# Performance work log

Measured on AMD Instinct MI355X. Metric: run time of the kernel, lower is better.

## Reference

```python
import jax, jax.numpy as jnp
import numpy as np

B, TE, TD = 16, 400, 64
E, H = 256, 512
H2 = 2 * H  # 1024
V = 32000


def setup_inputs():
    key = jax.random.key(0)
    k = jax.random.split(key, 16)
    s = 0.05
    return {
        "encoder_inputs": jax.random.randint(k[0], (B, TE), 0, V),
        "decoder_inputs": jax.random.randint(k[1], (B, TD), 0, V),
        "ext_oov_sizes": jax.random.randint(k[2], (B,), 0, 10),
        "enc_idxes_on_ext_voc": jax.random.randint(k[3], (B, TE), 0, V),
        "h0": jnp.zeros((2, B, H), jnp.float32),
        "c0": jnp.zeros((2, B, H), jnp.float32),
        "emb": jax.random.normal(k[4], (V, E)) * 0.1,
        "Wih_f": jax.random.normal(k[5], (4 * H, E)) * s,
        "Whh_f": jax.random.normal(k[6], (4 * H, H)) * s,
        "b_f": jnp.zeros((4 * H,), jnp.float32),
        "Wih_b": jax.random.normal(k[7], (4 * H, E)) * s,
        "Whh_b": jax.random.normal(k[8], (4 * H, H)) * s,
        "b_b": jnp.zeros((4 * H,), jnp.float32),
        "Wih_d": jax.random.normal(k[9], (4 * H2, E + 2 * H2)) * s,
        "Whh_d": jax.random.normal(k[10], (4 * H2, H2)) * s,
        "b_d": jnp.zeros((4 * H2,), jnp.float32),
        "W_ea": jax.random.normal(k[11], (H2, H2)) * 0.006,
        "W_da": jax.random.normal(k[12], (H2, H2)) * 0.006,
        "W_v": jax.random.normal(k[13], (V, 3 * H2)) * s,
        "b_v": jnp.zeros((V,), jnp.float32),
    }


def lstm_cell(x, h, c, Wih, Whh, b):
    z = x @ Wih.T + h @ Whh.T + b
    i, f, g, o = jnp.split(z, 4, axis=-1)
    i, f, o = jax.nn.sigmoid(i), jax.nn.sigmoid(f), jax.nn.sigmoid(o)
    c2 = f * c + i * jnp.tanh(g)
    return o * jnp.tanh(c2), c2


def run_lstm(xs, h0, c0, Wih, Whh, b):
    # xs: [T, B, E]
    def step(carry, x):
        h, c = lstm_cell(x, carry[0], carry[1], Wih, Whh, b)
        return (h, c), h
    (h, c), hs = jax.lax.scan(step, (h0, c0), xs)
    return hs, h, c


def _forward(emb, Wih_f, Whh_f, b_f, Wih_b, Whh_b, b_b, Wih_d, Whh_d, b_d,
             W_ea, W_da, W_v, b_v, h0, c0, encoder_inputs, decoder_inputs):
    xs = emb[encoder_inputs].transpose(1, 0, 2)  # [TE, B, E]
    hs_f, hf, cf = run_lstm(xs, h0[0], c0[0], Wih_f, Whh_f, b_f)
    hs_b, hb, cb = run_lstm(xs[::-1], h0[1], c0[1], Wih_b, Whh_b, b_b)
    enc_out = jnp.concatenate([hs_f, hs_b[::-1]], axis=-1).transpose(1, 0, 2)  # [B, TE, 2H]
    h = jnp.concatenate([hf, hb], axis=-1)  # [B, 2H] (torch reshape of bi-dir last hidden)
    c = jnp.concatenate([cf, cb], axis=-1)
    dec_emb = emb[decoder_inputs].transpose(1, 0, 2)  # [TD, B, E]

    def step(carry, xs_t):
        h, c, accum, buf = carry
        i, emb_t = xs_t
        # intra-temporal encoder attention: exp scores normalized by past accumulation
        scores = jnp.einsum('bd,btd->bt', h @ W_ea, enc_out)  # [B, TE]
        exp_s = jnp.exp(scores)
        denom = jnp.where(i == 0, jnp.ones_like(accum), accum)
        ep = exp_s / denom
        attn = ep / jnp.sum(ep, axis=-1, keepdims=True)
        ctx_e = jnp.einsum('bt,btd->bd', attn, enc_out)
        # intra-decoder attention over previously produced hidden states (masked)
        dsc = jnp.einsum('bd,tbd->bt', h @ W_da, buf)  # [B, TD]
        dsc = jnp.where((jnp.arange(TD) < i)[None, :], dsc, -1e30)
        dw = jnp.where(i == 0, 0.0, jax.nn.softmax(dsc, axis=-1))
        ctx_d = jnp.einsum('bt,tbd->bd', dw, buf)
        x = jnp.concatenate([emb_t, ctx_e, ctx_d], axis=-1)  # [B, E+4H]
        h2, c2 = lstm_cell(x, h, c, Wih_d, Whh_d, b_d)
        buf2 = buf.at[i].set(h2)
        feat = jnp.concatenate([h2, ctx_e, ctx_d], axis=-1)  # [B, 6H]
        logd = jax.nn.log_softmax(feat @ W_v.T + b_v, axis=-1)
        return (h2, c2, accum + exp_s, buf2), logd

    carry0 = (h, c, jnp.zeros((B, TE), h.dtype), jnp.zeros((TD, B, H2), h.dtype))
    (h, c, _, _), logds = jax.lax.scan(step, carry0, (jnp.arange(TD), dec_emb))
    return logds.transpose(1, 0, 2), h[None], c[None]


def reference(encoder_inputs, decoder_inputs, ext_oov_sizes, enc_idxes_on_ext_voc,
              h0, c0, emb, Wih_f, Whh_f, b_f, Wih_b, Whh_b, b_b,
              Wih_d, Whh_d, b_d, W_ea, W_da, W_v, b_v):
    # ext_oov_sizes / enc_idxes_on_ext_voc are unused by forward (as in the torch source)
    return _forward(emb, Wih_f, Whh_f, b_f, Wih_b, Whh_b, b_b, Wih_d, Whh_d, b_d,
                    W_ea, W_da, W_v, b_v, h0, c0, encoder_inputs, decoder_inputs)
```

## Files before the change

### kernel.cpp

```cpp
#include <hip/hip_runtime.h>
#include <math.h>

#define B_  16
#define TE_ 400
#define TD_ 64
#define E_  256
#define H_  512
#define H2_ 1024
#define V_  32000
#define KE_ 768

typedef __attribute__((ext_vector_type(4))) float f32x4;
typedef __attribute__((ext_vector_type(8))) short s16x8;
typedef __attribute__((ext_vector_type(8))) unsigned short u16x8;
typedef __attribute__((ext_vector_type(4))) unsigned short u16x4;

__device__ __forceinline__ float bf2f(unsigned short u){
  union { unsigned int i; float f; } v; v.i = ((unsigned int)u) << 16; return v.f;
}
__device__ __forceinline__ unsigned short f2bf(float f){
  union { float f; unsigned int i; } v; v.f = f;
  return (unsigned short)((v.i + 0x7fffu + ((v.i >> 16) & 1u)) >> 16);
}
__device__ __forceinline__ float sigmoidf_(float x){ return 1.f/(1.f + expf(-x)); }

__device__ __forceinline__ void gl_lds16(const void* gsrc, void* ldst){
  __builtin_amdgcn_global_load_lds(
      (const __attribute__((address_space(1))) unsigned int*)gsrc,
      (__attribute__((address_space(3))) unsigned int*)ldst, 16, 0, 0);
}

__device__ __forceinline__ void bar_arrive(unsigned* obj, unsigned widx){
  __syncthreads();
  if (threadIdx.x == 0){
    __threadfence();
    __hip_atomic_fetch_add(&obj[(widx & 7u)*32], 1u, __ATOMIC_RELAXED, __HIP_MEMORY_SCOPE_AGENT);
  }
}
__device__ __forceinline__ void bar_wait(unsigned* obj, unsigned nwg, unsigned widx, unsigned epoch){
  if (threadIdx.x == 0){
    if (widx == 0){
      for(;;){
        unsigned s = 0;
        #pragma unroll
        for (int k2 = 0; k2 < 8; ++k2)
          s += __hip_atomic_load(&obj[k2*32], __ATOMIC_RELAXED, __HIP_MEMORY_SCOPE_AGENT);
        if (s >= nwg*epoch) break;
      }
      __hip_atomic_store(&obj[256], epoch, __ATOMIC_RELEASE, __HIP_MEMORY_SCOPE_AGENT);
    } else {
      while (__hip_atomic_load(&obj[256], __ATOMIC_RELAXED, __HIP_MEMORY_SCOPE_AGENT) < epoch)
        __builtin_amdgcn_s_sleep(1);
    }
    __threadfence();
  }
  __syncthreads();
}
__device__ __forceinline__ void fast_bar(unsigned* obj, unsigned nwg, unsigned widx, unsigned epoch){
  bar_arrive(obj, widx);
  bar_wait(obj, nwg, widx, epoch);
}

__global__ void k_init(unsigned* bars, float* accum){
  int gid = blockIdx.x*256 + threadIdx.x;
  if (gid < 4096) bars[gid] = 0u;
  if (gid < B_*TE_) accum[gid] = 0.f;
}

__global__ void k_gather(const float* __restrict__ emb, const int* __restrict__ idx,
                         unsigned short* __restrict__ out, int T){
  int wv = threadIdx.x >> 6, l = threadIdx.x & 63;
  int row = blockIdx.x*4 + wv;
  if (row >= T*B_) return;
  int t = row >> 4, b = row & 15;
  int tok = idx[b*T + t];
  float4 v = *(const float4*)(emb + (size_t)tok*E_ + l*4);
  u16x4 o; o[0]=f2bf(v.x); o[1]=f2bf(v.y); o[2]=f2bf(v.z); o[3]=f2bf(v.w);
  *(u16x4*)(out + (size_t)row*E_ + l*4) = o;
}

__global__ void k_prep_enc(const float* __restrict__ Wih_f, const float* __restrict__ Whh_f,
                           const float* __restrict__ Wih_b, const float* __restrict__ Whh_b,
                           unsigned short* __restrict__ Wenc){
  int it = blockIdx.x*256 + threadIdx.x;
  int dir = it / (2048*96); int rem = it % (2048*96);
  int pr = rem / 96; int kc = rem % 96; int k0 = kc*8;
  int g = pr >> 6, r = pr & 63, gate = r >> 4, ul = r & 15;
  int orig = gate*H_ + g*16 + ul;
  const float* Wih = dir ? Wih_b : Wih_f;
  const float* Whh = dir ? Whh_b : Whh_f;
  u16x8 o;
  #pragma unroll
  for (int e = 0; e < 8; ++e){
    int k = k0 + e;
    float v = (k < E_) ? Wih[(size_t)orig*E_ + k] : Whh[(size_t)orig*H_ + (k - E_)];
    o[e] = f2bf(v);
  }
  *(u16x8*)(Wenc + ((size_t)dir*2048 + pr)*KE_ + k0) = o;
}

__global__ void k_prep_whext(const float* __restrict__ Whh_d, const float* __restrict__ W_da,
                             char* __restrict__ WhExt){
  int it = blockIdx.x*256 + threadIdx.x;
  if (it < 524288){
    int g = it >> 13; int rem = it & 8191;
    int kblk = rem >> 10; int rem2 = rem & 1023;
    int row = rem2 >> 4; int k8 = rem2 & 15;
    int gate = row >> 4, ul = row & 15;
    int orig = gate*H2_ + g*16 + ul;
    u16x8 o;
    #pragma unroll
    for (int e = 0; e < 8; ++e)
      o[e] = f2bf(Whh_d[(size_t)orig*H2_ + kblk*128 + k8*8 + e]);
    size_t off = (size_t)g*163840 + (size_t)kblk*20480 + (size_t)(row*256 + ((k8*16) ^ ((row&7)<<4)));
    *(u16x8*)(WhExt + off) = o;
  } else if (it < 655360){
    int qi = it - 524288;
    int g = qi >> 11; int rem = qi & 2047;
    int kblk = rem >> 8; int c2 = rem & 255;
    int wv = c2 >> 6, rr = (c2 >> 2) & 15, c = c2 & 3;
    u16x8 o;
    #pragma unroll
    for (int e = 0; e < 8; ++e)
      o[e] = f2bf(W_da[(size_t)(g*16 + rr)*H2_ + kblk*128 + wv*32 + c*8 + e]);
    size_t off = (size_t)g*163840 + (size_t)kblk*20480 + 16384 + (size_t)(wv*1024 + rr*64 + ((c*16) ^ ((rr&7)<<4)));
    *(u16x8*)(WhExt + off) = o;
  }
}

__global__ void k_prep_ctx(const float* __restrict__ Wih_d, char* __restrict__ CtxW){
  int it = blockIdx.x*256 + threadIdx.x;
  int g = it >> 14; int rem = it & 16383;
  int kblk = rem >> 10; int rem2 = rem & 1023;
  int row = rem2 >> 4; int k8 = rem2 & 15;
  int gate = row >> 4, ul = row & 15;
  int orig = gate*H2_ + g*16 + ul;
  int k = 256 + kblk*128 + k8*8;
  u16x8 o;
  #pragma unroll
  for (int e = 0; e < 8; ++e)
    o[e] = f2bf(Wih_d[(size_t)orig*2304 + k + e]);
  size_t off = (size_t)g*262144 + (size_t)kblk*16384 + (size_t)(row*256 + ((k8*16) ^ ((row&7)<<4)));
  *(u16x8*)(CtxW + off) = o;
}

__global__ void k_prep_wihemb(const float* __restrict__ Wih_d, unsigned short* __restrict__ Wemb){
  int it = blockIdx.x*256 + threadIdx.x;
  int p = it >> 5; int k0 = (it & 31)*8;
  int g = p >> 6, gate = (p >> 4) & 3, ul = p & 15;
  int orig = gate*H2_ + g*16 + ul;
  u16x8 o;
  #pragma unroll
  for (int e = 0; e < 8; ++e)
    o[e] = f2bf(Wih_d[(size_t)orig*2304 + k0 + e]);
  *(u16x8*)(Wemb + (size_t)p*256 + k0) = o;
}

__global__ void __launch_bounds__(256, 2) k_zinit(
    const unsigned short* __restrict__ A,
    const unsigned short* __restrict__ Bw,
    const float* __restrict__ bd,
    float* __restrict__ Cz)
{
  __shared__ unsigned short Ab[128*72];
  __shared__ unsigned short Bt[128*72];
  int p = blockIdx.x;
  int mt = p >> 5, nt = p & 31;
  int m0 = mt*128, n0 = nt*128;
  int tid = threadIdx.x, wvv = tid>>6, l = tid&63;
  int wr = wvv>>1, wc = wvv&1;
  f32x4 zero4 = {0.f,0.f,0.f,0.f};
  f32x4 acc[4][4];
  #pragma unroll
  for (int a=0;a<4;++a){
    #pragma unroll
    for (int b=0;b<4;++b) acc[a][b] = zero4;
  }
  for (int k0 = 0; k0 < 256; k0 += 64){
    #pragma unroll
    for (int qq = 0; qq < 4; ++qq){
      int idx8 = (tid + qq*256)*8;
      int r = idx8 >> 6, k = idx8 & 63;
      *(u16x8*)(Ab + r*72 + k) = *(const u16x8*)(A + (size_t)(m0+r)*256 + k0 + k);
      *(u16x8*)(Bt + r*72 + k) = *(const u16x8*)(Bw + (size_t)(n0+r)*256 + k0 + k);
    }
    __syncthreads();
    #pragma unroll
    for (int ks = 0; ks < 2; ++ks){
      s16x8 af[4], bf[4];
      #pragma unroll
      for (int fi=0;fi<4;++fi)
        af[fi] = *(const s16x8*)(Ab + (wr*64+fi*16+(l&15))*72 + ks*32 + (l>>4)*8);
      #pragma unroll
      for (int fj=0;fj<4;++fj)
        bf[fj] = *(const s16x8*)(Bt + (wc*64+fj*16+(l&15))*72 + ks*32 + (l>>4)*8);
      #pragma unroll
      for (int fi=0;fi<4;++fi){
        #pragma unroll
        for (int fj=0;fj<4;++fj)
          acc[fi][fj] = __builtin_amdgcn_mfma_f32_16x16x32_bf16(af[fi], bf[fj], acc[fi][fj], 0,0,0);
      }
    }
    __syncthreads();
  }
  #pragma unroll
  for (int fj=0;fj<4;++fj){
    int col = n0 + wc*64 + fj*16 + (l&15);
    int orig = ((col>>4)&3)*H2_ + (col>>6)*16 + (col&15);
    float bias = bd[orig];
    #pragma unroll
    for (int fi=0;fi<4;++fi){
      #pragma unroll
      for (int j=0;j<4;++j){
        int row = m0 + wr*64 + fi*16 + (l>>4)*4 + j;
        Cz[(size_t)row*4096 + col] = acc[fi][fj][j] + bias;
      }
    }
  }
}

__global__ void __launch_bounds__(256, 1) k_encoder(
    const unsigned short* __restrict__ xs,
    const unsigned short* __restrict__ Wenc,
    const float* __restrict__ b_f, const float* __restrict__ b_b,
    const float* __restrict__ h0, const float* __restrict__ c0,
    unsigned short* __restrict__ enc_out,
    unsigned short* __restrict__ hbuf,
    float* __restrict__ h0dec, float* __restrict__ c0dec,
    unsigned* __restrict__ bars)
{
  extern __shared__ char smem[];
  unsigned short* Wt = (unsigned short*)smem;
  unsigned short* At = Wt + 64*776;
  float* zl = (float*)(At + 16*776);
  int tid = threadIdx.x;
  int w = blockIdx.x;
  int dir = w >> 5, g = w & 31;
  int wv = tid >> 6, l = tid & 63;
  unsigned* bobj = bars + dir*512;
  {
    const unsigned short* Wsrc = Wenc + ((size_t)dir*2048 + g*64)*KE_;
    int r = tid >> 2, s = tid & 3;
    for (int c = 0; c < 24; ++c)
      *(u16x8*)(Wt + r*776 + s*192 + c*8) = *(const u16x8*)(Wsrc + (size_t)r*KE_ + s*192 + c*8);
  }
  const float* bias = dir ? b_b : b_f;
  int bb = tid >> 4, ul = tid & 15;
  float creg = c0[((size_t)dir*16 + bb)*H_ + g*16 + ul];
  int kchunk = (l >> 4) * 8;
  float bia = bias[wv*H_ + g*16 + (l&15)];
  f32x4 bias4 = { bia, bia, bia, bia };
  f32x4 zero4 = { 0.f, 0.f, 0.f, 0.f };
  {
    int r = tid >> 4, s = tid & 15;
    int tg0 = dir ? (TE_-1) : 0;
    *(u16x8*)(At + r*776 + s*16)     = *(const u16x8*)(xs + ((size_t)tg0*16 + r)*E_ + s*16);
    *(u16x8*)(At + r*776 + s*16 + 8) = *(const u16x8*)(xs + ((size_t)tg0*16 + r)*E_ + s*16 + 8);
    for (int e = 0; e < 32; ++e)
      At[r*776 + 256 + s*32 + e] = f2bf(h0[((size_t)dir*16 + r)*H_ + s*32 + e]);
  }
  __syncthreads();
  for (int t = 0; t < TE_; ++t){
    int tg = dir ? (TE_-1 - t) : t;
    f32x4 acc0 = bias4, acc1 = zero4;
    const unsigned short* brow = Wt + (wv*16 + (l&15))*776 + kchunk;
    const unsigned short* ap   = At + (l&15)*776 + kchunk;
    #pragma unroll
    for (int ks = 0; ks < 24; ++ks){
      s16x8 afr = *(const s16x8*)(ap + ks*32);
      s16x8 bfr = *(const s16x8*)(brow + ks*32);
      if (ks & 1) acc1 = __builtin_amdgcn_mfma_f32_16x16x32_bf16(afr, bfr, acc1, 0, 0, 0);
      else        acc0 = __builtin_amdgcn_mfma_f32_16x16x32_bf16(afr, bfr, acc0, 0, 0, 0);
    }
    f32x4 acc = acc0 + acc1;
    #pragma unroll
    for (int j = 0; j < 4; ++j)
      zl[wv*256 + ((l>>4)*4 + j)*16 + (l&15)] = acc[j];
    __syncthreads();
    float zi = zl[0*256 + bb*16 + ul];
    float zf = zl[1*256 + bb*16 + ul];
    float zg = zl[2*256 + bb*16 + ul];
    float zo = zl[3*256 + bb*16 + ul];
    float iv = sigmoidf_(zi), fv = sigmoidf_(zf), gv = tanhf(zg), ov = sigmoidf_(zo);
    float cc = fv*creg + iv*gv;
    float hh = ov * tanhf(cc);
    creg = cc;
    int u = g*16 + ul;
    unsigned short hb = f2bf(hh);
    hbuf[((size_t)dir*2 + ((t+1)&1))*(16*H_) + bb*H_ + u] = hb;
    enc_out[((size_t)bb*TE_ + tg)*H2_ + dir*H_ + u] = hb;
    if (t == TE_-1){
      h0dec[(size_t)bb*H2_ + dir*H_ + u] = hh;
      c0dec[(size_t)bb*H2_ + dir*H_ + u] = cc;
    }
    bar_arrive(bobj, (unsigned)g);
    if (t+1 < TE_){
      int r = tid >> 4, s = tid & 15;
      int tg2 = dir ? (TE_-2 - t) : (t+1);
      *(u16x8*)(At + r*776 + s*16)     = *(const u16x8*)(xs + ((size_t)tg2*16 + r)*E_ + s*16);
      *(u16x8*)(At + r*776 + s*16 + 8) = *(const u16x8*)(xs + ((size_t)tg2*16 + r)*E_ + s*16 + 8);
    }
    bar_wait(bobj, 32, (unsigned)g, (unsigned)(t+1));
    if (t+1 < TE_){
      int r = tid >> 4, s = tid & 15;
      const unsigned short* hsrc = hbuf + ((size_t)dir*2 + ((t+1)&1))*(16*H_) + r*H_ + s*32;
      for (int c = 0; c < 4; ++c)
        *(u16x8*)(At + r*776 + 256 + s*32 + c*8) = *(const u16x8*)(hsrc + c*8);
    }
    __syncthreads();
  }
}

__global__ void k_dec_init(const float* __restrict__ h0dec, unsigned short* __restrict__ hreg){
  int gid = blockIdx.x*256 + threadIdx.x;
  if (gid < 16384) hreg[gid] = f2bf(h0dec[gid]);
}

__global__ void __launch_bounds__(256, 2) k_penc(
    const unsigned short* __restrict__ enc,
    const float* __restrict__ Wea,
    unsigned short* __restrict__ P)
{
  __shared__ unsigned short Ab[128*72];
  __shared__ unsigned short Bt[128*72];
  int p = blockIdx.x;
  int mt = p >> 3, nt = p & 7;
  int m0 = mt*128, n0 = nt*128;
  int tid = threadIdx.x, wvv = tid>>6, l = tid&63;
  int wr = wvv>>1, wc = wvv&1;
  f32x4 zero4 = {0.f,0.f,0.f,0.f};
  f32x4 acc[4][4];
  #pragma unroll
  for (int a=0;a<4;++a){
    #pragma unroll
    for (int b=0;b<4;++b) acc[a][b] = zero4;
  }
  for (int k0 = 0; k0 < 1024; k0 += 64){
    #pragma unroll
    for (int qq = 0; qq < 4; ++qq){
      int idx8 = (tid + qq*256)*8;
      int r = idx8 >> 6, k = idx8 & 63;
      *(u16x8*)(Ab + r*72 + k) = *(const u16x8*)(enc + (size_t)(m0+r)*1024 + k0 + k);
    }
    #pragma unroll
    for (int qq = 0; qq < 4; ++qq){
      int idx8 = (tid + qq*256)*8;
      int r = idx8 >> 6, k = idx8 & 63;
      const float* src = Wea + (size_t)(n0+r)*1024 + k0 + k;
      float4 v0 = *(const float4*)src;
      float4 v1 = *(const float4*)(src+4);
      u16x8 o;
      o[0]=f2bf(v0.x); o[1]=f2bf(v0.y); o[2]=f2bf(v0.z); o[3]=f2bf(v0.w);
      o[4]=f2bf(v1.x); o[5]=f2bf(v1.y); o[6]=f2bf(v1.z); o[7]=f2bf(v1.w);
      *(u16x8*)(Bt + r*72 + k) = o;
    }
    __syncthreads();
    #pragma unroll
    for (int ks = 0; ks < 2; ++ks){
      s16x8 af[4], bf[4];
      #pragma unroll
      for (int fi=0;fi<4;++fi)
        af[fi] = *(const s16x8*)(Ab + (wr*64+fi*16+(l&15))*72 + ks*32 + (l>>4)*8);
      #pragma unroll
      for (int fj=0;fj<4;++fj)
        bf[fj] = *(const s16x8*)(Bt + (wc*64+fj*16+(l&15))*72 + ks*32 + (l>>4)*8);
      #pragma unroll
      for (int fi=0;fi<4;++fi){
        #pragma unroll
        for (int fj=0;fj<4;++fj)
          acc[fi][fj] = __builtin_amdgcn_mfma_f32_16x16x32_bf16(af[fi], bf[fj], acc[fi][fj], 0,0,0);
      }
    }
    __syncthreads();
  }
  #pragma unroll
  for (int fj=0;fj<4;++fj){
    int col = n0 + wc*64 + fj*16 + (l&15);
    #pragma unroll
    for (int fi=0;fi<4;++fi){
      #pragma unroll
      for (int j=0;j<4;++j){
        int row = m0 + wr*64 + fi*16 + (l>>4)*4 + j;
        P[(size_t)row*1024 + col] = f2bf(acc[fi][fj][j]);
      }
    }
  }
}

__device__ __forceinline__ void issueA(const char* gA, char* Bb, int wv, int l, int kblk, int buf){
  const char* gsrc = gA + (size_t)kblk*20480;
  char* lb = Bb + buf*20480;
  #pragma unroll
  for (int q = 0; q < 4; ++q)
    gl_lds16(gsrc + wv*4096 + q*1024 + (size_t)l*16, lb + wv*4096 + q*1024);
  gl_lds16(gsrc + 16384 + wv*1024 + (size_t)l*16, lb + 16384 + wv*1024);
}
__device__ __forceinline__ void issueC(const char* gC, char* Bb, int wv, int l, int kblk, int buf){
  const char* gsrc = gC + (size_t)kblk*16384;
  char* lb = Bb + buf*20480;
  #pragma unroll
  for (int q = 0; q < 4; ++q)
    gl_lds16(gsrc + wv*4096 + q*1024 + (size_t)l*16, lb + wv*4096 + q*1024);
}

__global__ void __launch_bounds__(256, 1) k_decoder(
  const char* __restrict__ WhExt,
  const char* __restrict__ CtxW,
  const float* __restrict__ zinit,
  const unsigned short* __restrict__ Penc,
  const unsigned short* __restrict__ enc_out,
  const float* __restrict__ c0dec,
  unsigned short* __restrict__ hreg,
  unsigned short* __restrict__ xbuf,
  float* __restrict__ q,
  float* __restrict__ accum,
  float* __restrict__ pctx,
  float* __restrict__ psum,
  unsigned short* __restrict__ bufh,
  unsigned short* __restrict__ Av,
  float* __restrict__ outHC,
  unsigned* __restrict__ bars)
{
  extern __shared__ char smem[];
  int tid = threadIdx.x, w = blockIdx.x;
  int wv = tid >> 6, l = tid & 63;
  unsigned* objA = bars + 1024;
  unsigned* objB = bars + 1536;
  unsigned* objC = bars + 2048;

  unsigned short* Atc = (unsigned short*)smem;
  unsigned short* Ah  = (unsigned short*)smem;
  char*  Bb = smem + 66560;
  float* zl = (float*)(smem + 148480);
  float* zq = (float*)(smem + 152576);
  unsigned short* encL = (unsigned short*)smem;
  float* epL  = (float*)(smem + 102400);
  float* dscL = (float*)(smem + 103424);

  bool isL = (w < 64);
  int eb = 0, ec = 0;
  if (w >= 64){ eb = (w-64) >> 3; ec = (w-64) & 7; }

  if (w >= 64){
    for (int rr = 0; rr < 50; ++rr){
      const unsigned short* src = enc_out + ((size_t)eb*TE_ + ec*50 + rr)*H2_;
      *(u16x4*)(encL + rr*1024 + tid*4) = *(const u16x4*)(src + tid*4);
    }
    __syncthreads();
  }
  float creg = 0.f;
  int bb = tid >> 4, ul = tid & 15;
  const char* gA = (const char*)WhExt + (size_t)w*163840;
  const char* gC = (const char*)CtxW + (size_t)w*262144;

  f32x4 acc0, acc1;

  for (int i = 0; i < TD_; ++i){
    if (isL){
      issueA(gA, Bb, wv, l, 0, 0);
      issueA(gA, Bb, wv, l, 1, 1);
      {
        int r = tid >> 4, s = tid & 15;
        const unsigned short* hsrc = hreg + (i&1)*16384 + r*H2_ + s*64;
        for (int c = 0; c < 8; ++c)
          *(u16x8*)(Ah + r*1032 + s*64 + c*8) = *(const u16x8*)(hsrc + c*8);
      }
      __syncthreads();
      {
        const float* zsrc = zinit + ((size_t)i*16 + (l>>4)*4)*4096 + w*64 + wv*16 + (l&15);
        f32x4 a; a[0]=zsrc[0]; a[1]=zsrc[4096]; a[2]=zsrc[8192]; a[3]=zsrc[12288];
        acc0 = a;
        f32x4 z4 = {0.f,0.f,0.f,0.f};
        acc1 = z4;
      }
      f32x4 accq = {0.f,0.f,0.f,0.f};
      int swz = ((l&7)<<4);
      for (int kblk = 0; kblk < 8; ++kblk){
        int buf = kblk % 3;
        if (kblk + 2 < 8) issueA(gA, Bb, wv, l, kblk+2, (kblk+2)%3);
        if (kblk < 6)       asm volatile("s_waitcnt vmcnt(10)" ::: "memory");
        else if (kblk == 6) asm volatile("s_waitcnt vmcnt(5)" ::: "memory");
        else                asm volatile("s_waitcnt vmcnt(0)" ::: "memory");
        const unsigned short* ap = Ah + (l&15)*1032 + kblk*128 + (l>>4)*8;
        const char* Bz = Bb + buf*20480 + wv*4096;
        #pragma unroll
        for (int ks = 0; ks < 4; ++ks){
          int k8 = ks*4 + (l>>4);
          s16x8 afr = *(const s16x8*)(ap + ks*32);
          s16x8 bfr = *(const s16x8*)(Bz + (l&15)*256 + ((k8*16) ^ swz));
          if (ks & 1) acc1 = __builtin_amdgcn_mfma_f32_16x16x32_bf16(afr, bfr, acc1, 0,0,0);
          else        acc0 = __builtin_amdgcn_mfma_f32_16x16x32_bf16(afr, bfr, acc0, 0,0,0);
        }
        {
          s16x8 afq = *(const s16x8*)(Ah + (l&15)*1032 + kblk*128 + wv*32 + (l>>4)*8);
          s16x8 bfq = *(const s16x8*)(Bb + buf*20480 + 16384 + wv*1024 + (l&15)*64 + ((((l>>4)*16)) ^ swz));
          accq = __builtin_amdgcn_mfma_f32_16x16x32_bf16(afq, bfq, accq, 0,0,0);
        }
      }
      #pragma unroll
      for (int j = 0; j < 4; ++j)
        zq[wv*256 + ((l>>4)*4+j)*16 + (l&15)] = accq[j];
      __syncthreads();
      float qv = zq[0*256 + bb*16 + ul] + zq[1*256 + bb*16 + ul]
               + zq[2*256 + bb*16 + ul] + zq[3*256 + bb*16 + ul];
      q[(size_t)bb*H2_ + w*16 + ul] = qv;
    } else {
      const unsigned short* hb_ = hreg + (i&1)*16384 + eb*H2_ + l*16;
      u16x8 hv0 = *(const u16x8*)hb_;
      u16x8 hv1 = *(const u16x8*)(hb_ + 8);
      float hf[16];
      #pragma unroll
      for (int c = 0; c < 8; ++c){ hf[c] = bf2f(hv0[c]); hf[8+c] = bf2f(hv1[c]); }
      for (int rr = wv; rr < 50; rr += 4){
        const unsigned short* pr = Penc + ((size_t)(eb*TE_ + ec*50 + rr))*H2_ + l*16;
        u16x8 p0 = *(const u16x8*)pr;
        u16x8 p1 = *(const u16x8*)(pr + 8);
        float sc = 0.f;
        #pragma unroll
        for (int c = 0; c < 8; ++c) sc += hf[c]*bf2f(p0[c]);
        #pragma unroll
        for (int c = 0; c < 8; ++c) sc += hf[8+c]*bf2f(p1[c]);
        #pragma unroll
        for (int o = 1; o < 64; o <<= 1) sc += __shfl_xor(sc, o);
        if (l == 0){
          int t = ec*50 + rr;
          float es = expf(sc);
          float aold = accum[eb*TE_ + t];
          float denom = (i == 0) ? 1.f : aold;
          accum[eb*TE_ + t] = aold + es;
          epL[rr] = es / denom;
        }
      }
      __syncthreads();
      float tot = 0.f;
      for (int rr = 0; rr < 50; ++rr) tot += epL[rr];
      float a0=0.f,a1=0.f,a2=0.f,a3=0.f;
      for (int rr = 0; rr < 50; ++rr){
        float wgt = epL[rr];
        u16x4 ev = *(const u16x4*)(encL + rr*1024 + tid*4);
        a0 += wgt*bf2f(ev[0]); a1 += wgt*bf2f(ev[1]); a2 += wgt*bf2f(ev[2]); a3 += wgt*bf2f(ev[3]);
      }
      int slot = w - 64;
      float4 o4; o4.x=a0; o4.y=a1; o4.z=a2; o4.w=a3;
      *(float4*)(pctx + (size_t)slot*1024 + tid*4) = o4;
      if (tid == 0) psum[slot] = tot;
      __syncthreads();
    }
    fast_bar(objA, 192, (unsigned)w, (unsigned)(i+1));

    if (isL){
      #pragma unroll
      for (int j = 0; j < 4; ++j)
        issueC(gC, Bb, wv, l, j, j);
    } else if (w < 96){
      int b = (w-64) >> 1, half = w & 1;
      int col = half*512 + tid*2;
      if (i == 0){
        *(unsigned*)(xbuf + (size_t)b*2048 + 1024 + col) = 0u;
        *(unsigned*)(Av + ((size_t)b*TD_ + i)*3072 + 2048 + col) = 0u;
      } else {
        const float* qp = q + (size_t)b*H2_ + l*16;
        float4 q0 = *(const float4*)(qp);
        float4 q1 = *(const float4*)(qp+4);
        float4 q2 = *(const float4*)(qp+8);
        float4 q3 = *(const float4*)(qp+12);
        for (int tp = wv; tp < i; tp += 4){
          const unsigned short* br = bufh + ((size_t)tp*16 + b)*H2_ + l*16;
          u16x8 e0 = *(const u16x8*)(br);
          u16x8 e1 = *(const u16x8*)(br + 8);
          float sc = q0.x*bf2f(e0[0]) + q0.y*bf2f(e0[1]) + q0.z*bf2f(e0[2]) + q0.w*bf2f(e0[3])
                   + q1.x*bf2f(e0[4]) + q1.y*bf2f(e0[5]) + q1.z*bf2f(e0[6]) + q1.w*bf2f(e0[7])
                   + q2.x*bf2f(e1[0]) + q2.y*bf2f(e1[1]) + q2.z*bf2f(e1[2]) + q2.w*bf2f(e1[3])
                   + q3.x*bf2f(e1[4]) + q3.y*bf2f(e1[5]) + q3.z*bf2f(e1[6]) + q3.w*bf2f(e1[7]);
          #pragma unroll
          for (int o = 1; o < 64; o <<= 1) sc += __shfl_xor(sc, o);
          if (l == 0) dscL[tp] = sc;
        }
        __syncthreads();
        float scv = (l < i) ? dscL[l] : -1e30f;
        float m = scv;
        #pragma unroll
        for (int o = 1; o < 64; o <<= 1) m = fmaxf(m, __shfl_xor(m, o));
        float e = (l < i) ? expf(scv - m) : 0.f;
        float ssum = e;
        #pragma unroll
        for (int o = 1; o < 64; o <<= 1) ssum += __shfl_xor(ssum, o);
        float wgt = e / ssum;
        float c0_ = 0.f, c1_ = 0.f;
        for (int tp = 0; tp < i; ++tp){
          float wt = __shfl(wgt, tp);
          unsigned hv = *(const unsigned*)(bufh + ((size_t)tp*16 + b)*H2_ + col);
          c0_ += wt*bf2f((unsigned short)hv);
          c1_ += wt*bf2f((unsigned short)(hv>>16));
        }
        unsigned o2 = (unsigned)f2bf(c0_) | ((unsigned)f2bf(c1_) << 16);
        *(unsigned*)(xbuf + (size_t)b*2048 + 1024 + col) = o2;
        *(unsigned*)(Av + ((size_t)b*TD_ + i)*3072 + 2048 + col) = o2;
      }
    } else if (w < 112){
      int b = w - 96;
      float sx=0.f, sy=0.f, sz=0.f, sw=0.f, pst=0.f;
      for (int c = 0; c < 8; ++c){
        float4 v = *(const float4*)(pctx + (size_t)(b*8+c)*1024 + tid*4);
        sx += v.x; sy += v.y; sz += v.z; sw += v.w;
        pst += psum[b*8+c];
      }
      float inv = 1.f/pst;
      u16x4 o; o[0]=f2bf(sx*inv); o[1]=f2bf(sy*inv); o[2]=f2bf(sz*inv); o[3]=f2bf(sw*inv);
      *(u16x4*)(xbuf + (size_t)b*2048 + tid*4) = o;
      *(u16x4*)(Av + ((size_t)b*TD_ + i)*3072 + 1024 + tid*4) = o;
    }
    fast_bar(objB, 192, (unsigned)w, (unsigned)(i+1));

    if (isL){
      {
        int r = tid >> 4, s = tid & 15;
        for (int c = 0; c < 16; ++c)
          *(u16x8*)(Atc + r*2056 + s*128 + c*8) = *(const u16x8*)(xbuf + (size_t)r*2048 + s*128 + c*8);
      }
      __syncthreads();
      int swz = ((l&7)<<4);
      for (int kblk = 0; kblk < 16; ++kblk){
        int buf = kblk & 3;
        if (kblk >= 4 && kblk <= 12) asm volatile("s_waitcnt vmcnt(12)" ::: "memory");
        else if (kblk == 13)         asm volatile("s_waitcnt vmcnt(8)" ::: "memory");
        else if (kblk == 14)         asm volatile("s_waitcnt vmcnt(4)" ::: "memory");
        else if (kblk == 15)         asm volatile("s_waitcnt vmcnt(0)" ::: "memory");
        const unsigned short* ap = Atc + (l&15)*2056 + kblk*128 + (l>>4)*8;
        const char* Bz = Bb + buf*20480 + wv*4096;
        #pragma unroll
        for (int ks = 0; ks < 4; ++ks){
          int k8 = ks*4 + (l>>4);
          s16x8 afr = *(const s16x8*)(ap + ks*32);
          s16x8 bfr = *(const s16x8*)(Bz + (l&15)*256 + ((k8*16) ^ swz));
          if (ks & 1) acc1 = __builtin_amdgcn_mfma_f32_16x16x32_bf16(afr, bfr, acc1, 0,0,0);
          else        acc0 = __builtin_amdgcn_mfma_f32_16x16x32_bf16(afr, bfr, acc0, 0,0,0);
        }
        if (kblk + 4 < 16) issueC(gC, Bb, wv, l, kblk+4, buf);
      }
      f32x4 acc = acc0 + acc1;
      #pragma unroll
      for (int j = 0; j < 4; ++j)
        zl[wv*256 + ((l>>4)*4+j)*16 + (l&15)] = acc[j];
      __syncthreads();
      float zi = zl[0*256 + bb*16 + ul];
      float zf = zl[1*256 + bb*16 + ul];
      float zg = zl[2*256 + bb*16 + ul];
      float zo = zl[3*256 + bb*16 + ul];
      if (i == 0) creg = c0dec[(size_t)bb*H2_ + w*16 + ul];
      float iv = sigmoidf_(zi), fv = sigmoidf_(zf), gv = tanhf(zg), ov = sigmoidf_(zo);
      float cc = fv*creg + iv*gv;
      float hh = ov*tanhf(cc);
      creg = cc;
      int u = w*16 + ul;
      unsigned short hb2 = f2bf(hh);
      hreg[((i+1)&1)*16384 + (size_t)bb*H2_ + u] = hb2;
      Av[((size_t)bb*TD_ + i)*3072 + u] = hb2;
      bufh[((size_t)i*16 + bb)*H2_ + u] = hb2;
      if (i == TD_-1){
        outHC[(size_t)bb*H2_ + u] = hh;
        outHC[16384 + (size_t)bb*H2_ + u] = cc;
      }
    }
    fast_bar(objC, 192, (unsigned)w, (unsigned)(i+1));
  }
}

__global__ void __launch_bounds__(256, 2) k_vocab_gemm(
    const unsigned short* __restrict__ Av,
    const float* __restrict__ Wv,
    const float* __restrict__ bv,
    float* __restrict__ out)
{
  __shared__ unsigned short Ab[128*72];
  __shared__ unsigned short Bt[128*72];
  int p = blockIdx.x;
  int mt = (p>>3)&7, nt = (p&7) + 8*(p>>6);
  if (nt >= 250) return;
  int m0 = mt*128, n0 = nt*128;
  int tid = threadIdx.x, wvv = tid>>6, l = tid&63;
  int wr = wvv>>1, wc = wvv&1;
  f32x4 zero4 = {0.f,0.f,0.f,0.f};
  f32x4 acc[4][4];
  #pragma unroll
  for (int a=0;a<4;++a){
    #pragma unroll
    for (int b=0;b<4;++b) acc[a][b] = zero4;
  }
  for (int k0 = 0; k0 < 3072; k0 += 64){
    #pragma unroll
    for (int qq = 0; qq < 4; ++qq){
      int idx8 = (tid + qq*256)*8;
      int r = idx8 >> 6, k = idx8 & 63;
      *(u16x8*)(Ab + r*72 + k) = *(const u16x8*)(Av + (size_t)(m0+r)*3072 + k0 + k);
    }
    #pragma unroll
    for (int qq = 0; qq < 4; ++qq){
      int idx8 = (tid + qq*256)*8;
      int r = idx8 >> 6, k = idx8 & 63;
      const float* src = Wv + (size_t)(n0+r)*3072 + k0 + k;
      float4 v0 = *(const float4*)src;
      float4 v1 = *(const float4*)(src+4);
      u16x8 o;
      o[0]=f2bf(v0.x); o[1]=f2bf(v0.y); o[2]=f2bf(v0.z); o[3]=f2bf(v0.w);
      o[4]=f2bf(v1.x); o[5]=f2bf(v1.y); o[6]=f2bf(v1.z); o[7]=f2bf(v1.w);
      *(u16x8*)(Bt + r*72 + k) = o;
    }
    __syncthreads();
    #pragma unroll
    for (int ks = 0; ks < 2; ++ks){
      s16x8 af[4], bf[4];
      #pragma unroll
      for (int fi=0;fi<4;++fi)
        af[fi] = *(const s16x8*)(Ab + (wr*64+fi*16+(l&15))*72 + ks*32 + (l>>4)*8);
      #pragma unroll
      for (int fj=0;fj<4;++fj)
        bf[fj] = *(const s16x8*)(Bt + (wc*64+fj*16+(l&15))*72 + ks*32 + (l>>4)*8);
      #pragma unroll
      for (int fi=0;fi<4;++fi){
        #pragma unroll
        for (int fj=0;fj<4;++fj)
          acc[fi][fj] = __builtin_amdgcn_mfma_f32_16x16x32_bf16(af[fi], bf[fj], acc[fi][fj], 0,0,0);
      }
    }
    __syncthreads();
  }
  #pragma unroll
  for (int fj=0;fj<4;++fj){
    int col = n0 + wc*64 + fj*16 + (l&15);
    float bias = bv[col];
    #pragma unroll
    for (int fi=0;fi<4;++fi){
      #pragma unroll
      for (int j=0;j<4;++j){
        int row = m0 + wr*64 + fi*16 + (l>>4)*4 + j;
        out[(size_t)row*V_ + col] = acc[fi][fj][j] + bias;
      }
    }
  }
}

__global__ void k_logsoftmax(float* __restrict__ out){
  int row = blockIdx.x;
  float* x = out + (size_t)row*V_;
  int tid = threadIdx.x;
  __shared__ float red[64];
  float m = -1e30f;
  for (int c = tid; c < V_; c += 256) m = fmaxf(m, x[c]);
  #pragma unroll
  for (int o=1;o<64;o<<=1) m = fmaxf(m, __shfl_xor(m,o));
  if ((tid&63)==0) red[tid>>6] = m;
  __syncthreads();
  m = fmaxf(fmaxf(red[0],red[1]), fmaxf(red[2],red[3]));
  float s = 0.f;
  for (int c = tid; c < V_; c += 256) s += expf(x[c]-m);
  #pragma unroll
  for (int o=1;o<64;o<<=1) s += __shfl_xor(s,o);
  if ((tid&63)==0) red[8 + (tid>>6)] = s;
  __syncthreads();
  s = red[8]+red[9]+red[10]+red[11];
  float lse = m + logf(s);
  for (int c = tid; c < V_; c += 256) x[c] = x[c] - lse;
}

extern "C" void kernel_launch(void* const* d_in, const int* in_sizes, int n_in,
                              void* d_out, int out_size, void* d_ws, size_t ws_size,
                              hipStream_t stream){
  (void)in_sizes; (void)n_in; (void)out_size; (void)ws_size;
  const int*   enc_in = (const int*)d_in[0];
  const int*   dec_in = (const int*)d_in[1];
  const float* h0   = (const float*)d_in[4];
  const float* c0   = (const float*)d_in[5];
  const float* emb  = (const float*)d_in[6];
  const float* Wih_f= (const float*)d_in[7];
  const float* Whh_f= (const float*)d_in[8];
  const float* b_f  = (const float*)d_in[9];
  const float* Wih_b= (const float*)d_in[10];
  const float* Whh_b= (const float*)d_in[11];
  const float* b_b  = (const float*)d_in[12];
  const float* Wih_d= (const float*)d_in[13];
  const float* Whh_d= (const float*)d_in[14];
  const float* b_d  = (const float*)d_in[15];
  const float* W_ea = (const float*)d_in[16];
  const float* W_da = (const float*)d_in[17];
  const float* W_v  = (const float*)d_in[18];
  const float* b_v  = (const float*)d_in[19];
  float* out = (float*)d_out;
  char* ws = (char*)d_ws;

  size_t o_bars   = 0;
  size_t o_accum  = 16384;
  size_t o_q      = o_accum + 25600;
  size_t o_xs     = o_q + 65536;
  size_t o_decemb = o_xs + (size_t)6400*256*2;
  size_t o_Wenc   = o_decemb + (size_t)1024*256*2;
  size_t o_WhExt  = o_Wenc + (size_t)2*2048*768*2;
  size_t o_CtxW   = o_WhExt + (size_t)64*163840;
  size_t o_Wemb   = o_CtxW + (size_t)64*262144;
  size_t o_zinit  = o_Wemb + (size_t)4096*256*2;
  size_t o_enc    = o_zinit + (size_t)1024*4096*4;
  size_t o_Penc   = o_enc + (size_t)16*400*1024*2;
  size_t o_hbuf   = o_Penc + (size_t)16*400*1024*2;
  size_t o_h0dec  = o_hbuf + (size_t)2*2*16*512*2;
  size_t o_c0dec  = o_h0dec + (size_t)16*1024*4;
  size_t o_hreg   = o_c0dec + (size_t)16*1024*4;
  size_t o_xbuf   = o_hreg + (size_t)2*16*1024*2;
  size_t o_pctx   = o_xbuf + (size_t)16*2048*2;
  size_t o_psum   = o_pctx + (size_t)128*1024*4;
  size_t o_bufh   = o_psum + 512;
  size_t o_Av     = o_bufh + (size_t)64*16*1024*2;

  unsigned* bars        = (unsigned*)(ws + o_bars);
  float* accum          = (float*)(ws + o_accum);
  float* q              = (float*)(ws + o_q);
  unsigned short* xs    = (unsigned short*)(ws + o_xs);
  unsigned short* decemb= (unsigned short*)(ws + o_decemb);
  unsigned short* Wenc  = (unsigned short*)(ws + o_Wenc);
  char* WhExt           = ws + o_WhExt;
  char* CtxW            = ws + o_CtxW;
  unsigned short* Wemb  = (unsigned short*)(ws + o_Wemb);
  float* zinit          = (float*)(ws + o_zinit);
  unsigned short* encO  = (unsigned short*)(ws + o_enc);
  unsigned short* Penc  = (unsigned short*)(ws + o_Penc);
  unsigned short* hbuf  = (unsigned short*)(ws + o_hbuf);
  float* h0dec          = (float*)(ws + o_h0dec);
  float* c0dec          = (float*)(ws + o_c0dec);
  unsigned short* hreg  = (unsigned short*)(ws + o_hreg);
  unsigned short* xbuf  = (unsigned short*)(ws + o_xbuf);
  float* pctx           = (float*)(ws + o_pctx);
  float* psum           = (float*)(ws + o_psum);
  unsigned short* bufh  = (unsigned short*)(ws + o_bufh);
  unsigned short* Av    = (unsigned short*)(ws + o_Av);

  hipFuncSetAttribute((const void*)k_encoder, hipFuncAttributeMaxDynamicSharedMemorySize, 131072);
  hipFuncSetAttribute((const void*)k_decoder, hipFuncAttributeMaxDynamicSharedMemorySize, 157696);

  k_init<<<26, 256, 0, stream>>>(bars, accum);
  k_gather<<<1600, 256, 0, stream>>>(emb, enc_in, xs, TE_);
  k_gather<<<256, 256, 0, stream>>>(emb, dec_in, decemb, TD_);
  k_prep_enc<<<1536, 256, 0, stream>>>(Wih_f, Whh_f, Wih_b, Whh_b, Wenc);
  k_prep_whext<<<2560, 256, 0, stream>>>(Whh_d, W_da, WhExt);
  k_prep_ctx<<<4096, 256, 0, stream>>>(Wih_d, CtxW);
  k_prep_wihemb<<<512, 256, 0, stream>>>(Wih_d, Wemb);
  k_zinit<<<256, 256, 0, stream>>>(decemb, Wemb, b_d, zinit);
  k_encoder<<<64, 256, 128512, stream>>>(xs, Wenc, b_f, b_b, h0, c0, encO, hbuf, h0dec, c0dec, bars);
  k_penc<<<400, 256, 0, stream>>>(encO, W_ea, Penc);
  k_dec_init<<<64, 256, 0, stream>>>(h0dec, hreg);
  k_decoder<<<192, 256, 156672, stream>>>(WhExt, CtxW, zinit, Penc, encO, c0dec,
                                          hreg, xbuf, q, accum, pctx, psum, bufh, Av,
                                          out + (size_t)32768000, bars);
  k_vocab_gemm<<<2048, 256, 0, stream>>>(Av, W_v, b_v, out);
  k_logsoftmax<<<1024, 256, 0, stream>>>(out);
}
```

Before: 6.342 ms.

## Fold encoder attention projection into decoder query, overlap weight prep with encoder

Removes the separate Penc GEMM over encoder outputs and instead projects the decoder state through W_ea each step, so attention scores are computed as enc_out·(W_ea^T·q). Weight-repacking kernels are folded into spare blocks of the encoder launch, which gets extra idle blocks so the packing overlaps the serial encoder recurrence. The encoder's and decoder's grid barriers are replaced with per-step counter barriers that need no reset. The context vector is accumulated atomically into a normalized buffer instead of a separate reduction phase. This trades a large up-front GEMM and extra launches for more per-step decoder work and more complex synchronization.

Measured after the change: 6.222 ms. Within noise of the previous version (-1.9%).

```diff
diff --git a/kernel.cpp b/kernel.cpp
--- a/kernel.cpp
+++ b/kernel.cpp
@@ -30,41 +30,30 @@
       (__attribute__((address_space(3))) unsigned int*)ldst, 16, 0, 0);
 }
 
-__device__ __forceinline__ void bar_arrive(unsigned* obj, unsigned widx){
+__device__ __forceinline__ void dec_bar(unsigned* inst, unsigned nwg){
   __syncthreads();
   if (threadIdx.x == 0){
     __threadfence();
-    __hip_atomic_fetch_add(&obj[(widx & 7u)*32], 1u, __ATOMIC_RELAXED, __HIP_MEMORY_SCOPE_AGENT);
-  }
-}
-__device__ __forceinline__ void bar_wait(unsigned* obj, unsigned nwg, unsigned widx, unsigned epoch){
-  if (threadIdx.x == 0){
-    if (widx == 0){
-      for(;;){
-        unsigned s = 0;
-        #pragma unroll
-        for (int k2 = 0; k2 < 8; ++k2)
-          s += __hip_atomic_load(&obj[k2*32], __ATOMIC_RELAXED, __HIP_MEMORY_SCOPE_AGENT);
-        if (s >= nwg*epoch) break;
-      }
-      __hip_atomic_store(&obj[256], epoch, __ATOMIC_RELEASE, __HIP_MEMORY_SCOPE_AGENT);
-    } else {
-      while (__hip_atomic_load(&obj[256], __ATOMIC_RELAXED, __HIP_MEMORY_SCOPE_AGENT) < epoch)
-        __builtin_amdgcn_s_sleep(1);
+    __hip_atomic_fetch_add(inst + (blockIdx.x & 15u)*16, 1u, __ATOMIC_RELAXED, __HIP_MEMORY_SCOPE_AGENT);
+    for(;;){
+      unsigned s = 0;
+      #pragma unroll
+      for (int k = 0; k < 16; ++k)
+        s += __hip_atomic_load(inst + k*16, __ATOMIC_RELAXED, __HIP_MEMORY_SCOPE_AGENT);
+      if (s >= nwg) break;
+      __builtin_amdgcn_s_sleep(1);
     }
     __threadfence();
   }
   __syncthreads();
 }
-__device__ __forceinline__ void fast_bar(unsigned* obj, unsigned nwg, unsigned widx, unsigned epoch){
-  bar_arrive(obj, widx);
-  bar_wait(obj, nwg, widx, epoch);
-}
-
-__global__ void k_init(unsigned* bars, float* accum){
+
+__global__ void k_init(unsigned* bars, float* accum, float* ctxn, float* psumT){
   int gid = blockIdx.x*256 + threadIdx.x;
-  if (gid < 4096) bars[gid] = 0u;
+  if (gid < 100352) bars[gid] = 0u;
   if (gid < B_*TE_) accum[gid] = 0.f;
+  if (gid < 16384) ctxn[gid] = 0.f;
+  if (gid < 16) psumT[gid] = 0.f;
 }
 
 __global__ void k_gather(const float* __restrict__ emb, const int* __restrict__ idx,
@@ -99,9 +88,10 @@
   *(u16x8*)(Wenc + ((size_t)dir*2048 + pr)*KE_ + k0) = o;
 }
 
-__global__ void k_prep_whext(const float* __restrict__ Whh_d, const float* __restrict__ W_da,
-                             char* __restrict__ WhExt){
-  int it = blockIdx.x*256 + threadIdx.x;
+__device__ __forceinline__ void prep_whext_item(int it, const float* __restrict__ Whh_d,
+                                                const float* __restrict__ W_da,
+                                                const float* __restrict__ W_ea,
+                                                char* __restrict__ WhExt){
   if (it < 524288){
     int g = it >> 13; int rem = it & 8191;
     int kblk = rem >> 10; int rem2 = rem & 1023;
@@ -112,24 +102,30 @@
     #pragma unroll
     for (int e = 0; e < 8; ++e)
       o[e] = f2bf(Whh_d[(size_t)orig*H2_ + kblk*128 + k8*8 + e]);
-    size_t off = (size_t)g*163840 + (size_t)kblk*20480 + (size_t)(row*256 + ((k8*16) ^ ((row&7)<<4)));
+    size_t off = (size_t)g*196608 + (size_t)kblk*24576 + (size_t)(row*256 + ((k8*16) ^ ((row&7)<<4)));
     *(u16x8*)(WhExt + off) = o;
-  } else if (it < 655360){
+  } else {
     int qi = it - 524288;
-    int g = qi >> 11; int rem = qi & 2047;
+    int which = qi >> 17;
+    int qj = qi & 131071;
+    int g = qj >> 11; int rem = qj & 2047;
     int kblk = rem >> 8; int c2 = rem & 255;
-    int wv = c2 >> 6, rr = (c2 >> 2) & 15, c = c2 & 3;
+    int wvv = c2 >> 6, rr = (c2 >> 2) & 15, c = c2 & 3;
+    const float* W = which ? W_ea : W_da;
     u16x8 o;
     #pragma unroll
-    for (int e = 0; e < 8; ++e)
-      o[e] = f2bf(W_da[(size_t)(g*16 + rr)*H2_ + kblk*128 + wv*32 + c*8 + e]);
-    size_t off = (size_t)g*163840 + (size_t)kblk*20480 + 16384 + (size_t)(wv*1024 + rr*64 + ((c*16) ^ ((rr&7)<<4)));
+    for (int e = 0; e < 8; ++e){
+      int k = kblk*128 + wvv*32 + c*8 + e;
+      o[e] = f2bf(W[(size_t)k*H2_ + g*16 + rr]);
+    }
+    size_t off = (size_t)g*196608 + (size_t)kblk*24576 + (which ? 20480 : 16384)
+               + (size_t)(wvv*1024 + rr*64 + ((c*16) ^ ((rr&3)<<4)));
     *(u16x8*)(WhExt + off) = o;
   }
 }
 
-__global__ void k_prep_ctx(const float* __restrict__ Wih_d, char* __restrict__ CtxW){
-  int it = blockIdx.x*256 + threadIdx.x;
+__device__ __forceinline__ void prep_ctx_item(int it, const float* __restrict__ Wih_d,
+                                              char* __restrict__ CtxW){
   int g = it >> 14; int rem = it & 16383;
   int kblk = rem >> 10; int rem2 = rem & 1023;
   int row = rem2 >> 4; int k8 = rem2 & 15;
@@ -227,17 +223,25 @@
     unsigned short* __restrict__ enc_out,
     unsigned short* __restrict__ hbuf,
     float* __restrict__ h0dec, float* __restrict__ c0dec,
-    unsigned* __restrict__ bars)
+    unsigned* __restrict__ bars,
+    const float* __restrict__ Whh_d, const float* __restrict__ W_da,
+    const float* __restrict__ W_ea, const float* __restrict__ Wih_d,
+    char* __restrict__ WhExt, char* __restrict__ CtxW)
 {
   extern __shared__ char smem[];
+  int tid = threadIdx.x;
+  int w = blockIdx.x;
+  if (w >= 64){
+    int base = (w - 64)*256 + tid;
+    for (int it = base; it < 786432; it += 36864) prep_whext_item(it, Whh_d, W_da, W_ea, WhExt);
+    for (int it = base; it < 1048576; it += 36864) prep_ctx_item(it, Wih_d, CtxW);
+    return;
+  }
   unsigned short* Wt = (unsigned short*)smem;
   unsigned short* At = Wt + 64*776;
   float* zl = (float*)(At + 16*776);
-  int tid = threadIdx.x;
-  int w = blockIdx.x;
   int dir = w >> 5, g = w & 31;
   int wv = tid >> 6, l = tid & 63;
-  unsigned* bobj = bars + dir*512;
   {
     const unsigned short* Wsrc = Wenc + ((size_t)dir*2048 + g*64)*KE_;
     int r = tid >> 2, s = tid & 3;
@@ -293,14 +297,30 @@
       h0dec[(size_t)bb*H2_ + dir*H_ + u] = hh;
       c0dec[(size_t)bb*H2_ + dir*H_ + u] = cc;
     }
-    bar_arrive(bobj, (unsigned)g);
+    unsigned* cnt = bars + (size_t)(dir*400 + t)*64;
+    __syncthreads();
+    if (tid == 0){
+      __threadfence();
+      __hip_atomic_fetch_add(cnt + (g&3)*16, 1u, __ATOMIC_RELAXED, __HIP_MEMORY_SCOPE_AGENT);
+    }
     if (t+1 < TE_){
       int r = tid >> 4, s = tid & 15;
       int tg2 = dir ? (TE_-2 - t) : (t+1);
       *(u16x8*)(At + r*776 + s*16)     = *(const u16x8*)(xs + ((size_t)tg2*16 + r)*E_ + s*16);
       *(u16x8*)(At + r*776 + s*16 + 8) = *(const u16x8*)(xs + ((size_t)tg2*16 + r)*E_ + s*16 + 8);
     }
-    bar_wait(bobj, 32, (unsigned)g, (unsigned)(t+1));
+    if (tid == 0){
+      for(;;){
+        unsigned s_ = 0;
+        #pragma unroll
+        for (int k2 = 0; k2 < 4; ++k2)
+          s_ += __hip_atomic_load(cnt + k2*16, __ATOMIC_RELAXED, __HIP_MEMORY_SCOPE_AGENT);
+        if (s_ >= 32) break;
+        __builtin_amdgcn_s_sleep(1);
+      }
+      __threadfence();
+    }
+    __syncthreads();
     if (t+1 < TE_){
       int r = tid >> 4, s = tid & 15;
       const unsigned short* hsrc = hbuf + ((size_t)dir*2 + ((t+1)&1))*(16*H_) + r*H_ + s*32;
@@ -316,88 +336,18 @@
   if (gid < 16384) hreg[gid] = f2bf(h0dec[gid]);
 }
 
-__global__ void __launch_bounds__(256, 2) k_penc(
-    const unsigned short* __restrict__ enc,
-    const float* __restrict__ Wea,
-    unsigned short* __restrict__ P)
-{
-  __shared__ unsigned short Ab[128*72];
-  __shared__ unsigned short Bt[128*72];
-  int p = blockIdx.x;
-  int mt = p >> 3, nt = p & 7;
-  int m0 = mt*128, n0 = nt*128;
-  int tid = threadIdx.x, wvv = tid>>6, l = tid&63;
-  int wr = wvv>>1, wc = wvv&1;
-  f32x4 zero4 = {0.f,0.f,0.f,0.f};
-  f32x4 acc[4][4];
-  #pragma unroll
-  for (int a=0;a<4;++a){
-    #pragma unroll
-    for (int b=0;b<4;++b) acc[a][b] = zero4;
-  }
-  for (int k0 = 0; k0 < 1024; k0 += 64){
-    #pragma unroll
-    for (int qq = 0; qq < 4; ++qq){
-      int idx8 = (tid + qq*256)*8;
-      int r = idx8 >> 6, k = idx8 & 63;
-      *(u16x8*)(Ab + r*72 + k) = *(const u16x8*)(enc + (size_t)(m0+r)*1024 + k0 + k);
-    }
-    #pragma unroll
-    for (int qq = 0; qq < 4; ++qq){
-      int idx8 = (tid + qq*256)*8;
-      int r = idx8 >> 6, k = idx8 & 63;
-      const float* src = Wea + (size_t)(n0+r)*1024 + k0 + k;
-      float4 v0 = *(const float4*)src;
-      float4 v1 = *(const float4*)(src+4);
-      u16x8 o;
-      o[0]=f2bf(v0.x); o[1]=f2bf(v0.y); o[2]=f2bf(v0.z); o[3]=f2bf(v0.w);
-      o[4]=f2bf(v1.x); o[5]=f2bf(v1.y); o[6]=f2bf(v1.z); o[7]=f2bf(v1.w);
-      *(u16x8*)(Bt + r*72 + k) = o;
-    }
-    __syncthreads();
-    #pragma unroll
-    for (int ks = 0; ks < 2; ++ks){
-      s16x8 af[4], bf[4];
-      #pragma unroll
-      for (int fi=0;fi<4;++fi)
-        af[fi] = *(const s16x8*)(Ab + (wr*64+fi*16+(l&15))*72 + ks*32 + (l>>4)*8);
-      #pragma unroll
-      for (int fj=0;fj<4;++fj)
-        bf[fj] = *(const s16x8*)(Bt + (wc*64+fj*16+(l&15))*72 + ks*32 + (l>>4)*8);
-      #pragma unroll
-      for (int fi=0;fi<4;++fi){
-        #pragma unroll
-        for (int fj=0;fj<4;++fj)
-          acc[fi][fj] = __builtin_amdgcn_mfma_f32_16x16x32_bf16(af[fi], bf[fj], acc[fi][fj], 0,0,0);
-      }
-    }
-    __syncthreads();
-  }
-  #pragma unroll
-  for (int fj=0;fj<4;++fj){
-    int col = n0 + wc*64 + fj*16 + (l&15);
-    #pragma unroll
-    for (int fi=0;fi<4;++fi){
-      #pragma unroll
-      for (int j=0;j<4;++j){
-        int row = m0 + wr*64 + fi*16 + (l>>4)*4 + j;
-        P[(size_t)row*1024 + col] = f2bf(acc[fi][fj][j]);
-      }
-    }
-  }
-}
-
 __device__ __forceinline__ void issueA(const char* gA, char* Bb, int wv, int l, int kblk, int buf){
-  const char* gsrc = gA + (size_t)kblk*20480;
-  char* lb = Bb + buf*20480;
+  const char* gsrc = gA + (size_t)kblk*24576;
+  char* lb = Bb + buf*24576;
   #pragma unroll
   for (int q = 0; q < 4; ++q)
     gl_lds16(gsrc + wv*4096 + q*1024 + (size_t)l*16, lb + wv*4096 + q*1024);
   gl_lds16(gsrc + 16384 + wv*1024 + (size_t)l*16, lb + 16384 + wv*1024);
+  gl_lds16(gsrc + 20480 + wv*1024 + (size_t)l*16, lb + 20480 + wv*1024);
 }
 __device__ __forceinline__ void issueC(const char* gC, char* Bb, int wv, int l, int kblk, int buf){
   const char* gsrc = gC + (size_t)kblk*16384;
-  char* lb = Bb + buf*20480;
+  char* lb = Bb + buf*16384;
   #pragma unroll
   for (int q = 0; q < 4; ++q)
     gl_lds16(gsrc + wv*4096 + q*1024 + (size_t)l*16, lb + wv*4096 + q*1024);
@@ -407,15 +357,14 @@
   const char* __restrict__ WhExt,
   const char* __restrict__ CtxW,
   const float* __restrict__ zinit,
-  const unsigned short* __restrict__ Penc,
   const unsigned short* __restrict__ enc_out,
   const float* __restrict__ c0dec,
   unsigned short* __restrict__ hreg,
   unsigned short* __restrict__ xbuf,
   float* __restrict__ q,
   float* __restrict__ accum,
-  float* __restrict__ pctx,
-  float* __restrict__ psum,
+  float* __restrict__ ctxn,
+  float* __restrict__ psumT,
   unsigned short* __restrict__ bufh,
   unsigned short* __restrict__ Av,
   float* __restrict__ outHC,
@@ -424,24 +373,23 @@
   extern __shared__ char smem[];
   int tid = threadIdx.x, w = blockIdx.x;
   int wv = tid >> 6, l = tid & 63;
-  unsigned* objA = bars + 1024;
-  unsigned* objB = bars + 1536;
-  unsigned* objC = bars + 2048;
+  unsigned* dbase = bars + 51200;
 
   unsigned short* Atc = (unsigned short*)smem;
   unsigned short* Ah  = (unsigned short*)smem;
   char*  Bb = smem + 66560;
-  float* zl = (float*)(smem + 148480);
-  float* zq = (float*)(smem + 152576);
+  float* zl = (float*)(smem + 140288);
+  float* zq = (float*)(smem + 144384);
   unsigned short* encL = (unsigned short*)smem;
   float* epL  = (float*)(smem + 102400);
-  float* dscL = (float*)(smem + 103424);
-
-  bool isL = (w < 64);
+  float* dscL = (float*)smem;
+
+  bool isZ = (w < 64);
+  bool isE = (w >= 64 && w < 192);
   int eb = 0, ec = 0;
-  if (w >= 64){ eb = (w-64) >> 3; ec = (w-64) & 7; }
-
-  if (w >= 64){
+  if (isE){ eb = (w-64) >> 3; ec = (w-64) & 7; }
+
+  if (isE){
     for (int rr = 0; rr < 50; ++rr){
       const unsigned short* src = enc_out + ((size_t)eb*TE_ + ec*50 + rr)*H2_;
       *(u16x4*)(encL + rr*1024 + tid*4) = *(const u16x4*)(src + tid*4);
@@ -450,13 +398,17 @@
   }
   float creg = 0.f;
   int bb = tid >> 4, ul = tid & 15;
-  const char* gA = (const char*)WhExt + (size_t)w*163840;
-  const char* gC = (const char*)CtxW + (size_t)w*262144;
+  const char* gA = WhExt + (size_t)w*196608;
+  const char* gC = CtxW + (size_t)w*262144;
 
   f32x4 acc0, acc1;
 
   for (int i = 0; i < TD_; ++i){
-    if (isL){
+    if (isZ){
+      const float* zsrc = zinit + ((size_t)i*16 + (l>>4)*4)*4096 + w*64 + wv*16 + (l&15);
+      f32x4 a0i; a0i[0]=zsrc[0]; a0i[1]=zsrc[4096]; a0i[2]=zsrc[8192]; a0i[3]=zsrc[12288];
+      ctxn[w*256 + tid] = 0.f;
+      if (w == 0 && tid < 16) psumT[tid] = 0.f;
       issueA(gA, Bb, wv, l, 0, 0);
       issueA(gA, Bb, wv, l, 1, 1);
       {
@@ -466,23 +418,20 @@
           *(u16x8*)(Ah + r*1032 + s*64 + c*8) = *(const u16x8*)(hsrc + c*8);
       }
       __syncthreads();
-      {
-        const float* zsrc = zinit + ((size_t)i*16 + (l>>4)*4)*4096 + w*64 + wv*16 + (l&15);
-        f32x4 a; a[0]=zsrc[0]; a[1]=zsrc[4096]; a[2]=zsrc[8192]; a[3]=zsrc[12288];
-        acc0 = a;
-        f32x4 z4 = {0.f,0.f,0.f,0.f};
-        acc1 = z4;
-      }
-      f32x4 accq = {0.f,0.f,0.f,0.f};
+      acc0 = a0i;
+      f32x4 z4 = {0.f,0.f,0.f,0.f};
+      acc1 = z4;
+      f32x4 accq = z4, accqe = z4;
       int swz = ((l&7)<<4);
+      int swzq = ((l&3)<<4);
       for (int kblk = 0; kblk < 8; ++kblk){
         int buf = kblk % 3;
         if (kblk + 2 < 8) issueA(gA, Bb, wv, l, kblk+2, (kblk+2)%3);
-        if (kblk < 6)       asm volatile("s_waitcnt vmcnt(10)" ::: "memory");
-        else if (kblk == 6) asm volatile("s_waitcnt vmcnt(5)" ::: "memory");
+        if (kblk < 6)       asm volatile("s_waitcnt vmcnt(12)" ::: "memory");
+        else if (kblk == 6) asm volatile("s_waitcnt vmcnt(6)" ::: "memory");
         else                asm volatile("s_waitcnt vmcnt(0)" ::: "memory");
         const unsigned short* ap = Ah + (l&15)*1032 + kblk*128 + (l>>4)*8;
-        const char* Bz = Bb + buf*20480 + wv*4096;
+        const char* Bz = Bb + buf*24576 + wv*4096;
         #pragma unroll
         for (int ks = 0; ks < 4; ++ks){
           int k8 = ks*4 + (l>>4);
@@ -491,35 +440,49 @@
           if (ks & 1) acc1 = __builtin_amdgcn_mfma_f32_16x16x32_bf16(afr, bfr, acc1, 0,0,0);
           else        acc0 = __builtin_amdgcn_mfma_f32_16x16x32_bf16(afr, bfr, acc0, 0,0,0);
         }
-        {
-          s16x8 afq = *(const s16x8*)(Ah + (l&15)*1032 + kblk*128 + wv*32 + (l>>4)*8);
-          s16x8 bfq = *(const s16x8*)(Bb + buf*20480 + 16384 + wv*1024 + (l&15)*64 + ((((l>>4)*16)) ^ swz));
-          accq = __builtin_amdgcn_mfma_f32_16x16x32_bf16(afq, bfq, accq, 0,0,0);
-        }
-      }
+        s16x8 afq = *(const s16x8*)(Ah + (l&15)*1032 + kblk*128 + wv*32 + (l>>4)*8);
+        s16x8 bfq = *(const s16x8*)(Bb + buf*24576 + 16384 + wv*1024 + (l&15)*64 + ((((l>>4)*16)) ^ swzq));
+        accq = __builtin_amdgcn_mfma_f32_16x16x32_bf16(afq, bfq, accq, 0,0,0);
+        s16x8 bfe = *(const s16x8*)(Bb + buf*24576 + 20480 + wv*1024 + (l&15)*64 + ((((l>>4)*16)) ^ swzq));
+        accqe = __builtin_amdgcn_mfma_f32_16x16x32_bf16(afq, bfe, accqe, 0,0,0);
+      }
+      #pragma unroll
+      for (int j = 0; j < 4; ++j){
+        zq[wv*256 + ((l>>4)*4+j)*16 + (l&15)] = accq[j];
+        zq[1024 + wv*256 + ((l>>4)*4+j)*16 + (l&15)] = accqe[j];
+      }
+      __syncthreads();
+      float qd = zq[0*256 + bb*16 + ul] + zq[1*256 + bb*16 + ul]
+               + zq[2*256 + bb*16 + ul] + zq[3*256 + bb*16 + ul];
+      q[16384 + (size_t)bb*1024 + w*16 + ul] = qd;
+      float qe = zq[1024 + 0*256 + bb*16 + ul] + zq[1024 + 1*256 + bb*16 + ul]
+               + zq[1024 + 2*256 + bb*16 + ul] + zq[1024 + 3*256 + bb*16 + ul];
+      q[(size_t)bb*1024 + w*16 + ul] = qe;
+    }
+    dec_bar(dbase + (size_t)(0*64 + i)*256, 208);
+
+    if (isZ){
       #pragma unroll
       for (int j = 0; j < 4; ++j)
-        zq[wv*256 + ((l>>4)*4+j)*16 + (l&15)] = accq[j];
-      __syncthreads();
-      float qv = zq[0*256 + bb*16 + ul] + zq[1*256 + bb*16 + ul]
-               + zq[2*256 + bb*16 + ul] + zq[3*256 + bb*16 + ul];
-      q[(size_t)bb*H2_ + w*16 + ul] = qv;
-    } else {
-      const unsigned short* hb_ = hreg + (i&1)*16384 + eb*H2_ + l*16;
-      u16x8 hv0 = *(const u16x8*)hb_;
-      u16x8 hv1 = *(const u16x8*)(hb_ + 8);
-      float hf[16];
-      #pragma unroll
-      for (int c = 0; c < 8; ++c){ hf[c] = bf2f(hv0[c]); hf[8+c] = bf2f(hv1[c]); }
+        issueC(gC, Bb, wv, l, j, j);
+    } else if (isE){
+      const float* qp = q + (size_t)eb*1024 + l*16;
+      float4 q0 = *(const float4*)(qp);
+      float4 q1 = *(const float4*)(qp+4);
+      float4 q2 = *(const float4*)(qp+8);
+      float4 q3 = *(const float4*)(qp+12);
+      float qf[16];
+      qf[0]=q0.x;qf[1]=q0.y;qf[2]=q0.z;qf[3]=q0.w; qf[4]=q1.x;qf[5]=q1.y;qf[6]=q1.z;qf[7]=q1.w;
+      qf[8]=q2.x;qf[9]=q2.y;qf[10]=q2.z;qf[11]=q2.w; qf[12]=q3.x;qf[13]=q3.y;qf[14]=q3.z;qf[15]=q3.w;
       for (int rr = wv; rr < 50; rr += 4){
-        const unsigned short* pr = Penc + ((size_t)(eb*TE_ + ec*50 + rr))*H2_ + l*16;
-        u16x8 p0 = *(const u16x8*)pr;
-        u16x8 p1 = *(const u16x8*)(pr + 8);
+        const unsigned short* er = encL + rr*1024 + l*16;
+        u16x8 e0 = *(const u16x8*)(er);
+        u16x8 e1 = *(const u16x8*)(er + 8);
         float sc = 0.f;
         #pragma unroll
-        for (int c = 0; c < 8; ++c) sc += hf[c]*bf2f(p0[c]);
-        #pragma unroll
-        for (int c = 0; c < 8; ++c) sc += hf[8+c]*bf2f(p1[c]);
+        for (int c = 0; c < 8; ++c) sc += qf[c]*bf2f(e0[c]);
+        #pragma unroll
+        for (int c = 0; c < 8; ++c) sc += qf[8+c]*bf2f(e1[c]);
         #pragma unroll
         for (int o = 1; o < 64; o <<= 1) sc += __shfl_xor(sc, o);
         if (l == 0){
@@ -540,26 +503,18 @@
         u16x4 ev = *(const u16x4*)(encL + rr*1024 + tid*4);
         a0 += wgt*bf2f(ev[0]); a1 += wgt*bf2f(ev[1]); a2 += wgt*bf2f(ev[2]); a3 += wgt*bf2f(ev[3]);
       }
-      int slot = w - 64;
-      float4 o4; o4.x=a0; o4.y=a1; o4.z=a2; o4.w=a3;
-      *(float4*)(pctx + (size_t)slot*1024 + tid*4) = o4;
-      if (tid == 0) psum[slot] = tot;
-      __syncthreads();
-    }
-    fast_bar(objA, 192, (unsigned)w, (unsigned)(i+1));
-
-    if (isL){
-      #pragma unroll
-      for (int j = 0; j < 4; ++j)
-        issueC(gC, Bb, wv, l, j, j);
-    } else if (w < 96){
-      int b = (w-64) >> 1, half = w & 1;
-      int col = half*512 + tid*2;
+      float* dst = ctxn + (size_t)eb*1024 + tid*4;
+      atomicAdd(dst+0, a0); atomicAdd(dst+1, a1); atomicAdd(dst+2, a2); atomicAdd(dst+3, a3);
+      if (tid == 0) atomicAdd(psumT + eb, tot);
+    } else {
+      int b = w - 192;
+      int col = tid*4;
       if (i == 0){
-        *(unsigned*)(xbuf + (size_t)b*2048 + 1024 + col) = 0u;
-        *(unsigned*)(Av + ((size_t)b*TD_ + i)*3072 + 2048 + col) = 0u;
+        u16x4 z4v = {0,0,0,0};
+        *(u16x4*)(xbuf + (size_t)b*1024 + col) = z4v;
+        *(u16x4*)(Av + ((size_t)b*TD_ + i)*3072 + 2048 + col) = z4v;
       } else {
-        const float* qp = q + (size_t)b*H2_ + l*16;
+        const float* qp = q + 16384 + (size_t)b*1024 + l*16;
         float4 q0 = *(const float4*)(qp);
         float4 q1 = *(const float4*)(qp+4);
         float4 q2 = *(const float4*)(qp+8);
@@ -586,37 +541,39 @@
         #pragma unroll
         for (int o = 1; o < 64; o <<= 1) ssum += __shfl_xor(ssum, o);
         float wgt = e / ssum;
-        float c0_ = 0.f, c1_ = 0.f;
+        float c0_=0.f,c1_=0.f,c2_=0.f,c3_=0.f;
         for (int tp = 0; tp < i; ++tp){
           float wt = __shfl(wgt, tp);
-          unsigned hv = *(const unsigned*)(bufh + ((size_t)tp*16 + b)*H2_ + col);
-          c0_ += wt*bf2f((unsigned short)hv);
-          c1_ += wt*bf2f((unsigned short)(hv>>16));
+          u16x4 hv = *(const u16x4*)(bufh + ((size_t)tp*16 + b)*H2_ + col);
+          c0_ += wt*bf2f(hv[0]); c1_ += wt*bf2f(hv[1]); c2_ += wt*bf2f(hv[2]); c3_ += wt*bf2f(hv[3]);
         }
-        unsigned o2 = (unsigned)f2bf(c0_) | ((unsigned)f2bf(c1_) << 16);
-        *(unsigned*)(xbuf + (size_t)b*2048 + 1024 + col) = o2;
-        *(unsigned*)(Av + ((size_t)b*TD_ + i)*3072 + 2048 + col) = o2;
-      }
-    } else if (w < 112){
-      int b = w - 96;
-      float sx=0.f, sy=0.f, sz=0.f, sw=0.f, pst=0.f;
-      for (int c = 0; c < 8; ++c){
-        float4 v = *(const float4*)(pctx + (size_t)(b*8+c)*1024 + tid*4);
-        sx += v.x; sy += v.y; sz += v.z; sw += v.w;
-        pst += psum[b*8+c];
-      }
-      float inv = 1.f/pst;
-      u16x4 o; o[0]=f2bf(sx*inv); o[1]=f2bf(sy*inv); o[2]=f2bf(sz*inv); o[3]=f2bf(sw*inv);
-      *(u16x4*)(xbuf + (size_t)b*2048 + tid*4) = o;
-      *(u16x4*)(Av + ((size_t)b*TD_ + i)*3072 + 1024 + tid*4) = o;
-    }
-    fast_bar(objB, 192, (unsigned)w, (unsigned)(i+1));
-
-    if (isL){
+        u16x4 o4; o4[0]=f2bf(c0_); o4[1]=f2bf(c1_); o4[2]=f2bf(c2_); o4[3]=f2bf(c3_);
+        *(u16x4*)(xbuf + (size_t)b*1024 + col) = o4;
+        *(u16x4*)(Av + ((size_t)b*TD_ + i)*3072 + 2048 + col) = o4;
+      }
+    }
+    dec_bar(dbase + (size_t)(1*64 + i)*256, 208);
+
+    if (isZ){
       {
         int r = tid >> 4, s = tid & 15;
-        for (int c = 0; c < 16; ++c)
-          *(u16x8*)(Atc + r*2056 + s*128 + c*8) = *(const u16x8*)(xbuf + (size_t)r*2048 + s*128 + c*8);
+        float inv = 1.f / psumT[r];
+        const float* cn = ctxn + (size_t)r*1024 + s*64;
+        for (int c8 = 0; c8 < 8; ++c8){
+          float4 v0 = *(const float4*)(cn + c8*8);
+          float4 v1 = *(const float4*)(cn + c8*8 + 4);
+          u16x8 o;
+          o[0]=f2bf(v0.x*inv); o[1]=f2bf(v0.y*inv); o[2]=f2bf(v0.z*inv); o[3]=f2bf(v0.w*inv);
+          o[4]=f2bf(v1.x*inv); o[5]=f2bf(v1.y*inv); o[6]=f2bf(v1.z*inv); o[7]=f2bf(v1.w*inv);
+          *(u16x8*)(Atc + r*2056 + s*64 + c8*8) = o;
+        }
+        const unsigned short* xd = xbuf + (size_t)r*1024 + s*64;
+        for (int c8 = 0; c8 < 8; ++c8)
+          *(u16x8*)(Atc + r*2056 + 1024 + s*64 + c8*8) = *(const u16x8*)(xd + c8*8);
+      }
+      {
+        float val = ctxn[(size_t)bb*1024 + w*16 + ul] / psumT[bb];
+        Av[((size_t)bb*TD_ + i)*3072 + 1024 + w*16 + ul] = f2bf(val);
       }
       __syncthreads();
       int swz = ((l&7)<<4);
@@ -627,7 +584,7 @@
         else if (kblk == 14)         asm volatile("s_waitcnt vmcnt(4)" ::: "memory");
         else if (kblk == 15)         asm volatile("s_waitcnt vmcnt(0)" ::: "memory");
         const unsigned short* ap = Atc + (l&15)*2056 + kblk*128 + (l>>4)*8;
-        const char* Bz = Bb + buf*20480 + wv*4096;
+        const char* Bz = Bb + buf*16384 + wv*4096;
         #pragma unroll
         for (int ks = 0; ks < 4; ++ks){
           int k8 = ks*4 + (l>>4);
@@ -662,7 +619,7 @@
         outHC[16384 + (size_t)bb*H2_ + u] = cc;
       }
     }
-    fast_bar(objC, 192, (unsigned)w, (unsigned)(i+1));
+    dec_bar(dbase + (size_t)(2*64 + i)*256, 208);
   }
 }
 
@@ -789,30 +746,31 @@
   char* ws = (char*)d_ws;
 
   size_t o_bars   = 0;
-  size_t o_accum  = 16384;
+  size_t o_accum  = 409600;
   size_t o_q      = o_accum + 25600;
-  size_t o_xs     = o_q + 65536;
+  size_t o_ctxn   = o_q + 131072;
+  size_t o_psumT  = o_ctxn + 65536;
+  size_t o_xs     = o_psumT + 256;
   size_t o_decemb = o_xs + (size_t)6400*256*2;
   size_t o_Wenc   = o_decemb + (size_t)1024*256*2;
   size_t o_WhExt  = o_Wenc + (size_t)2*2048*768*2;
-  size_t o_CtxW   = o_WhExt + (size_t)64*163840;
+  size_t o_CtxW   = o_WhExt + (size_t)64*196608;
   size_t o_Wemb   = o_CtxW + (size_t)64*262144;
   size_t o_zinit  = o_Wemb + (size_t)4096*256*2;
   size_t o_enc    = o_zinit + (size_t)1024*4096*4;
-  size_t o_Penc   = o_enc + (size_t)16*400*1024*2;
-  size_t o_hbuf   = o_Penc + (size_t)16*400*1024*2;
+  size_t o_hbuf   = o_enc + (size_t)16*400*1024*2;
   size_t o_h0dec  = o_hbuf + (size_t)2*2*16*512*2;
   size_t o_c0dec  = o_h0dec + (size_t)16*1024*4;
   size_t o_hreg   = o_c0dec + (size_t)16*1024*4;
   size_t o_xbuf   = o_hreg + (size_t)2*16*1024*2;
-  size_t o_pctx   = o_xbuf + (size_t)16*2048*2;
-  size_t o_psum   = o_pctx + (size_t)128*1024*4;
-  size_t o_bufh   = o_psum + 512;
+  size_t o_bufh   = o_xbuf + (size_t)16*1024*2;
   size_t o_Av     = o_bufh + (size_t)64*16*1024*2;
 
   unsigned* bars        = (unsigned*)(ws + o_bars);
   float* accum          = (float*)(ws + o_accum);
   float* q              = (float*)(ws + o_q);
+  float* ctxn           = (float*)(ws + o_ctxn);
+  float* psumT          = (float*)(ws + o_psumT);
   unsigned short* xs    = (unsigned short*)(ws + o_xs);
   unsigned short* decemb= (unsigned short*)(ws + o_decemb);
   unsigned short* Wenc  = (unsigned short*)(ws + o_Wenc);
@@ -821,33 +779,29 @@
   unsigned short* Wemb  = (unsigned short*)(ws + o_Wemb);
   float* zinit          = (float*)(ws + o_zinit);
   unsigned short* encO  = (unsigned short*)(ws + o_enc);
-  unsigned short* Penc  = (unsigned short*)(ws + o_Penc);
   unsigned short* hbuf  = (unsigned short*)(ws + o_hbuf);
   float* h0dec          = (float*)(ws + o_h0dec);
   float* c0dec          = (float*)(ws + o_c0dec);
   unsigned short* hreg  = (unsigned short*)(ws + o_hreg);
   unsigned short* xbuf  = (unsigned short*)(ws + o_xbuf);
-  float* pctx           = (float*)(ws + o_pctx);
-  float* psum           = (float*)(ws + o_psum);
-  unsigned short* bufh  = (unsigned short*)(ws + o_bufh);
+  float* bufh_          = (float*)(ws + o_bufh);
   unsigned short* Av    = (unsigned short*)(ws + o_Av);
 
   hipFuncSetAttribute((const void*)k_encoder, hipFuncAttributeMaxDynamicSharedMemorySize, 131072);
-  hipFuncSetAttribute((const void*)k_decoder, hipFuncAttributeMaxDynamicSharedMemorySize, 157696);
-
-  k_init<<<26, 256, 0, stream>>>(bars, accum);
+  hipFuncSetAttribute((const void*)k_decoder, hipFuncAttributeMaxDynamicSharedMemorySize, 152576);
+
+  k_init<<<392, 256, 0, stream>>>(bars, accum, ctxn, psumT);
   k_gather<<<1600, 256, 0, stream>>>(emb, enc_in, xs, TE_);
   k_gather<<<256, 256, 0, stream>>>(emb, dec_in, decemb, TD_);
   k_prep_enc<<<1536, 256, 0, stream>>>(Wih_f, Whh_f, Wih_b, Whh_b, Wenc);
-  k_prep_whext<<<2560, 256, 0, stream>>>(Whh_d, W_da, WhExt);
-  k_prep_ctx<<<4096, 256, 0, stream>>>(Wih_d, CtxW);
   k_prep_wihemb<<<512, 256, 0, stream>>>(Wih_d, Wemb);
   k_zinit<<<256, 256, 0, stream>>>(decemb, Wemb, b_d, zinit);
-  k_encoder<<<64, 256, 128512, stream>>>(xs, Wenc, b_f, b_b, h0, c0, encO, hbuf, h0dec, c0dec, bars);
-  k_penc<<<400, 256, 0, stream>>>(encO, W_ea, Penc);
+  k_encoder<<<208, 256, 128512, stream>>>(xs, Wenc, b_f, b_b, h0, c0, encO, hbuf, h0dec, c0dec, bars,
+                                          Whh_d, W_da, W_ea, Wih_d, WhExt, CtxW);
   k_dec_init<<<64, 256, 0, stream>>>(h0dec, hreg);
-  k_decoder<<<192, 256, 156672, stream>>>(WhExt, CtxW, zinit, Penc, encO, c0dec,
-                                          hreg, xbuf, q, accum, pctx, psum, bufh, Av,
+  k_decoder<<<208, 256, 152576, stream>>>(WhExt, CtxW, zinit, encO, c0dec,
+                                          hreg, xbuf, q, accum, ctxn, psumT,
+                                          (unsigned short*)bufh_, Av,
                                           out + (size_t)32768000, bars);
   k_vocab_gemm<<<2048, 256, 0, stream>>>(Av, W_v, b_v, out);
   k_logsoftmax<<<1024, 256, 0, stream>>>(out);
```
